# Optimization experiments

Hardware: AMD Instinct MI355X
Metric: run time of the kernel (lower is better)

Reference implementation:

```python
import jax, jax.numpy as jnp
import numpy as np
from jax.ops import segment_sum, segment_max

ALPHA = 0.01  # leaky relu slope

def _cmul(a, b):
    # complex multiply on last-axis (re, im) pairs
    re = a[..., 0] * b[..., 0] - a[..., 1] * b[..., 1]
    im = a[..., 0] * b[..., 1] + a[..., 1] * b[..., 0]
    return jnp.stack((re, im), axis=-1)

def setup_inputs() -> dict:
    key = jax.random.key(0)
    ks = jax.random.split(key, 8)
    N, D, M, E, L, H, R, FH = 50000, 64, 3, 100000, 4, 8, 5, 128
    return {
        "features": jax.random.normal(ks[0], (N, D), jnp.float32),
        "attn1_w": jax.random.normal(ks[1], (M, H, D), jnp.float32) * 0.1,
        "attn2":   jax.random.normal(ks[2], (M, H, D), jnp.float32) * 0.1,
        "r_vec":   jax.random.normal(ks[3], (R, D // 2, 2), jnp.float32),
        "proj_w1": jax.random.normal(ks[4], (FH, H * D), jnp.float32) * 0.05,
        "proj_b1": jnp.zeros((FH,), jnp.float32),
        "proj_w2": jax.random.normal(ks[5], (1, FH), jnp.float32) * 0.1,
        "inst":    jax.random.randint(ks[6], (M, E, L), 0, N),
        "etypes":  jax.random.randint(ks[7], (M, L - 1), 0, 2 * R, dtype=jnp.int32),
    }

def reference(features, attn1_w, attn2, r_vec, proj_w1, proj_b1, proj_w2, inst, etypes):
    N, D = features.shape
    M, E, L = inst.shape
    H = attn1_w.shape[1]
    # --- conjugate-augmented, L2-normalized relation rotations ([2R, D/2, 2]) ---
    rn = r_vec / jnp.linalg.norm(r_vec, axis=2, keepdims=True)
    conj = rn * jnp.array([1.0, -1.0], rn.dtype)
    r_full = jnp.stack((rn, conj), axis=1).reshape(2 * r_vec.shape[0], r_vec.shape[1], 2)

    node_embs = []  # per-metapath [N, H*D]
    for m in range(M):
        # SemanticEncoder: gather + rotation recurrence + mean over path positions
        edata = features[inst[m]]                       # [E, L, D]
        edc = edata.reshape(E, L, D // 2, 2)
        # final_r_vec: backward cumulative complex product; position L-1 = identity
        ident = jnp.concatenate(
            [jnp.ones((D // 2, 1), edata.dtype), jnp.zeros((D // 2, 1), edata.dtype)], axis=-1)
        fr = [None] * L
        fr[L - 1] = ident
        for i in range(L - 2, -1, -1):
            fr[i] = _cmul(fr[i + 1], r_full[etypes[m, i]])
        fr = jnp.stack(fr, axis=0)                      # [L, D/2, 2]
        rotated = _cmul(edc, fr[None])                  # [E, L, D/2, 2] (pos L-1 rotated by identity)
        me = rotated.reshape(E, L, D).mean(axis=1)      # metapath embedding [E, D]

        # MessageAggregator: GAT-style segment softmax over instances per dst node
        dst = inst[m, :, 0]                             # [E]
        a1 = features[dst] @ attn1_w[m].T               # [E, H]
        a2 = jnp.einsum('ed,hd->eh', me, attn2[m])      # [E, H]
        a = jax.nn.leaky_relu(a1 + a2, ALPHA)           # [E, H]
        amax = segment_max(a, dst, num_segments=N)      # [N, H]
        amax = jnp.where(jnp.isfinite(amax), amax, 0.0)
        ex = jnp.exp(a - amax[dst])                     # [E, H]
        den = segment_sum(ex, dst, num_segments=N)      # [N, H]
        attn = ex / jnp.where(den[dst] > 0, den[dst], 1.0)
        agg = segment_sum(attn[:, :, None] * me[:, None, :], dst, num_segments=N)  # [N, H, D]
        node_embs.append(jax.nn.elu(agg).reshape(N, H * D))

    # Subgraph_Fusion: semantic attention over metapaths
    z = jnp.stack(node_embs, axis=1)                    # [N, M, H*D]
    w = jnp.tanh(z @ proj_w1.T + proj_b1) @ proj_w2.T   # [N, M, 1]
    beta = jax.nn.softmax(w.mean(axis=0), axis=0)       # [M, 1]
    out = (beta[None] * z).sum(axis=1)                  # [N, H*D]
    return out
```

## Files before the change

### kernel.cpp

```cpp
#include <hip/hip_runtime.h>
#include <hip/hip_bf16.h>
#include <hip/hip_fp16.h>
#include <math.h>

#define NN 50000
#define DD 64
#define MM 3
#define EE 100000
#define LL 4
#define HH 8
#define FHH 128
#define HD 512
#define NROWS (NN*MM)
#define LRELU_ALPHA 0.01f

#define WSUM_BINS 256
#define WSUM_SZ (MM*WSUM_BINS)
#define BINS (MM*NN)
#define NBLK ((BINS + 1023)/1024)
#define GT_TILE 224

#define OFF_ZB    0
#define OFF_WSUM  (NROWS*HD/2)
#define OFF_BETA  (OFF_WSUM + WSUM_SZ)
#define OFF_W1BF  (OFF_BETA + 16)
#define OFF_WU    (OFF_W1BF + 32768)
#define OFF_FRS   (OFF_WU + 6144)
#define OFF_GT    (OFF_FRS + 768)
#define OFF_INTS  (OFF_GT + MM*NN*32)
#define IOFF_CNT    0
#define IOFF_CURSOR (IOFF_CNT + BINS)
#define IOFF_PART   (IOFF_CURSOR + BINS)
#define IOFF_BSUM   (IOFF_PART + BINS)
#define IOFF_BTOP   (IOFF_BSUM + 256)
#define IOFF_SEGC   (IOFF_BTOP + 256)
#define IOFF_REC    (IOFF_SEGC + 2*BINS)
#define INTS_END    (IOFF_REC + 4*MM*EE)
#define OFF_F16   (OFF_INTS + INTS_END)

typedef short v8s __attribute__((ext_vector_type(8)));
typedef float v4f __attribute__((ext_vector_type(4)));

__device__ __forceinline__ float elu_f(float x) {
    return x > 0.f ? x : (__expf(x) - 1.f);
}

__device__ __forceinline__ float tanh_fast(float x) {
    float e = __expf(2.f * x);
    return 1.f - 2.f / (e + 1.f);
}

__device__ __forceinline__ unsigned int pk_bf16x2(float x, float y) {
    float2 f2; f2.x = x; f2.y = y;
    __hip_bfloat162 h = __float22bfloat162_rn(f2);
    union { __hip_bfloat162 h; unsigned int u; } cv;
    cv.h = h;
    return cv.u;
}

__device__ __forceinline__ float bf_lo(unsigned int u) {
    union { unsigned int x; float f; } c; c.x = u << 16; return c.f;
}
__device__ __forceinline__ float bf_hi(unsigned int u) {
    union { unsigned int x; float f; } c; c.x = u & 0xffff0000u; return c.f;
}

__device__ __forceinline__ float2 h2f(unsigned int u) {
    union { unsigned int x; __half2 h; } c; c.x = u;
    return __half22float2(c.h);
}

__device__ __forceinline__ void build_frs(
    float frs[LL][DD/2][2], const float* r_vec, const int* etypes, int m, int t)
{
    if (t < DD/2) {
        float cr = 1.f, ci = 0.f;
        frs[LL-1][t][0] = 1.f; frs[LL-1][t][1] = 0.f;
        for (int i = LL-2; i >= 0; --i) {
            int et = etypes[m*(LL-1) + i];
            float rr = r_vec[((et>>1)*(DD/2) + t)*2 + 0];
            float ri = r_vec[((et>>1)*(DD/2) + t)*2 + 1];
            float inv = rsqrtf(rr*rr + ri*ri);
            rr *= inv; ri *= inv;
            if (et & 1) ri = -ri;
            float nr = cr*rr - ci*ri;
            float ni = cr*ri + ci*rr;
            cr = nr; ci = ni;
            frs[i][t][0] = cr; frs[i][t][1] = ci;
        }
    }
}

__global__ __launch_bounds__(256) void fcvt_kernel(
    const float* __restrict__ f, ushort* __restrict__ f16)
{
    int i = blockIdx.x*256 + threadIdx.x;
    float4 v = ((const float4*)f)[i];
    __half2 h0 = __float22half2_rn(make_float2(v.x, v.y));
    __half2 h1 = __float22half2_rn(make_float2(v.z, v.w));
    union { __half2 h; unsigned int u; } c0, c1;
    c0.h = h0; c1.h = h1;
    ((uint2*)f16)[i] = make_uint2(c0.u, c1.u);
}


__global__ __launch_bounds__(256) void hist_kernel(
    const int* __restrict__ inst, int* __restrict__ cnt)
{
    int e = blockIdx.x*256 + threadIdx.x;
    int m = blockIdx.y;
    if (e >= EE) return;
    int dst = inst[((size_t)m*EE + e)*LL];
    atomicAdd(&cnt[m*NN + dst], 1);
}

__global__ __launch_bounds__(256) void scan_partial_kernel(
    const int* __restrict__ cnt, int* __restrict__ part, int* __restrict__ bsum)
{
    __shared__ int sd[256];
    const int t = threadIdx.x;
    const int base = blockIdx.x*1024 + t*4;
    int v0=0,v1=0,v2=0,v3=0;
    if (base+3 < BINS) {
        int4 v = *(const int4*)&cnt[base];
        v0=v.x; v1=v.y; v2=v.z; v3=v.w;
    } else {
        if (base+0 < BINS) v0 = cnt[base+0];
        if (base+1 < BINS) v1 = cnt[base+1];
        if (base+2 < BINS) v2 = cnt[base+2];
        if (base+3 < BINS) v3 = cnt[base+3];
    }
    int tot = v0+v1+v2+v3;
    sd[t] = tot; __syncthreads();
    #pragma unroll
    for (int off = 1; off < 256; off <<= 1) {
        int val = (t >= off) ? sd[t-off] : 0;
        __syncthreads();
        sd[t] += val;
        __syncthreads();
    }
    int excl = sd[t] - tot;
    if (base+0 < BINS) part[base+0] = excl;
    if (base+1 < BINS) part[base+1] = excl + v0;
    if (base+2 < BINS) part[base+2] = excl + v0 + v1;
    if (base+3 < BINS) part[base+3] = excl + v0 + v1 + v2;
    if (t == 255) bsum[blockIdx.x] = sd[255];
}

__global__ __launch_bounds__(256) void scan_tops_kernel(
    const int* __restrict__ bsum, int* __restrict__ btop)
{
    __shared__ int sd[256];
    const int t = threadIdx.x;
    int v = (t < NBLK) ? bsum[t] : 0;
    sd[t] = v; __syncthreads();
    #pragma unroll
    for (int off = 1; off < 256; off <<= 1) {
        int val = (t >= off) ? sd[t-off] : 0;
        __syncthreads();
        sd[t] += val;
        __syncthreads();
    }
    if (t < NBLK) btop[t] = sd[t] - v;
}

__global__ __launch_bounds__(256) void fixup_kernel(
    int* __restrict__ part, const int* __restrict__ btop,
    const int* __restrict__ cnt, int2* __restrict__ segc)
{
    int i = blockIdx.x*256 + threadIdx.x;
    if (i >= BINS) return;
    int p = part[i] + btop[i >> 10];
    part[i] = p;
    segc[i] = make_int2(p, cnt[i]);
}

__global__ __launch_bounds__(256) void scatter_kernel(
    const int4* __restrict__ inst4, const int* __restrict__ part,
    int* __restrict__ cursor, int4* __restrict__ rec)
{
    int e = blockIdx.x*256 + threadIdx.x;
    int m = blockIdx.y;
    if (e >= EE) return;
    int4 v = inst4[(size_t)m*EE + e];
    int bin = m*NN + v.x;
    int pos = part[bin] + atomicAdd(&cursor[bin], 1);
    rec[pos] = make_int4(v.y, v.z, v.w, 0);
}

__global__ __launch_bounds__(64) void ugen_kernel(
    const float* __restrict__ r_vec,
    const int* __restrict__ etypes,
    const float* __restrict__ attn1_w,
    const float* __restrict__ attn2,
    float* __restrict__ Wu,
    float* __restrict__ frs_pk)
{
    const int m = blockIdx.x;
    __shared__ float frs[LL][DD/2][2];
    const int t = threadIdx.x;
    build_frs(frs, r_vec, etypes, m, t);
    __syncthreads();
    if (t < 32) {
        float4 v0, v1;
        v0.x = frs[0][t][0]; v0.y = frs[0][t][1];
        v0.z = frs[1][t][0]; v0.w = frs[1][t][1];
        v1.x = frs[2][t][0]; v1.y = frs[2][t][1];
        v1.z = frs[3][t][0]; v1.w = frs[3][t][1];
        ((float4*)frs_pk)[(m*32 + t)*2 + 0] = v0;
        ((float4*)frs_pk)[(m*32 + t)*2 + 1] = v1;
    }
    for (int idx = t; idx < 32*64; idx += 64) {
        int j = idx >> 6, d = idx & 63, p = d >> 1;
        int l = (j < 8) ? 0 : (j >> 3);
        int h = j & 7;
        float fr = frs[l][p][0], fi = frs[l][p][1];
        float w2r = attn2[m*HD + h*DD + 2*p];
        float w2i = attn2[m*HD + h*DD + 2*p + 1];
        float u = (d & 1) ? (fr*w2i - fi*w2r) : (fr*w2r + fi*w2i);
        float val = 0.25f * u + ((j < 8) ? attn1_w[m*HD + h*DD + d] : 0.f);
        Wu[(m*32 + j)*64 + d] = val;
    }
}

__global__ __launch_bounds__(256) void gt_kernel(
    const float* __restrict__ features,
    const float* __restrict__ Wu,
    float* __restrict__ gt)
{
    __shared__ float xs[GT_TILE*65];
    const int m = blockIdx.y;
    const int node0 = blockIdx.x * GT_TILE;
    const int t = threadIdx.x;
    #pragma unroll
    for (int i = 0; i < 14; ++i) {
        int idx = t + 256*i;
        int r = idx >> 4, c4 = idx & 15;
        int gr = node0 + r;
        float4 v = make_float4(0.f,0.f,0.f,0.f);
        if (gr < NN) v = ((const float4*)features)[gr*16 + c4];
        float* dst = &xs[r*65 + c4*4];
        dst[0]=v.x; dst[1]=v.y; dst[2]=v.z; dst[3]=v.w;
    }
    __syncthreads();
    if (t >= GT_TILE) return;
    int node = node0 + t;
    float acc[32];
    #pragma unroll
    for (int j=0;j<32;++j) acc[j]=0.f;
    const float* Wm = Wu + m*2048;
    for (int d = 0; d < 64; ++d) {
        float x = xs[t*65 + d];
        #pragma unroll
        for (int j = 0; j < 32; ++j)
            acc[j] += x * Wm[j*64 + d];
    }
    if (node < NN) {
        float* o = gt + ((size_t)m*NN + node)*32;
        #pragma unroll
        for (int j4 = 0; j4 < 8; ++j4) {
            float4 v; v.x=acc[j4*4]; v.y=acc[j4*4+1]; v.z=acc[j4*4+2]; v.w=acc[j4*4+3];
            ((float4*)o)[j4] = v;
        }
    }
}

__global__ __launch_bounds__(256) void node_kernel(
    const unsigned int* __restrict__ f16u,
    const float* __restrict__ frs_pk,
    const int4*  __restrict__ rec4,
    const int2*  __restrict__ segc,
    const float* __restrict__ gt,
    ushort* __restrict__ Zb)
{
    const int m = blockIdx.y;
    const int t = threadIdx.x;
    const int lane = t & 63;
    const int hl   = lane & 31;
    const int half = lane >> 5;
    const int wid  = t >> 6;
    const int node = blockIdx.x*4 + wid;

    const int bin = m*NN + node;
    ushort* zrow = Zb + ((size_t)node*MM + m)*HD;
    const int2 sc = segc[bin];
    const int start = sc.x, ecnt = sc.y;
    if (ecnt == 0) {
        ((uint4*)zrow)[lane] = make_uint4(0u,0u,0u,0u);
        return;
    }

    const float4* fp = (const float4*)frs_pk + ((size_t)m*32 + hl)*2;
    const float4 fA = fp[0], fB = fp[1];
    const float f0x=fA.x, f0y=fA.y, f1x=fA.z, f1y=fA.w;
    const float f2x=fB.x, f2y=fB.y, f3x=fB.z, f3y=fB.w;

    float2 x0 = h2f(f16u[(size_t)node*32 + hl]);
    const float me0r = x0.x*f0x - x0.y*f0y;
    const float me0i = x0.x*f0y + x0.y*f0x;

    const float c0 = (hl < HH) ? gt[(size_t)bin*32 + hl] : 0.f;
    const int lsel = hl >> 3;
    const bool gm = (hl >= 8);
    const float* gtm = gt + (size_t)m*NN*32;

    float accr[HH], acci[HH];
    #pragma unroll
    for (int h = 0; h < HH; ++h) { accr[h] = 0.f; acci[h] = 0.f; }
    float den = 0.f;

    for (int q = 0; q < ecnt; q += 2) {
        int myq = q + half;
        bool valid = (myq < ecnt);
        int qq = valid ? myq : (ecnt - 1);
        int4 r = rec4[start + qq];
        int i1 = r.x, i2 = r.y, i3 = r.z;

        int idxg = (lsel == 1) ? i1 : ((lsel == 2) ? i2 : i3);
        float gv = 0.f;
        if (gm) gv = gtm[(size_t)idxg*32 + hl];

        unsigned int u1 = f16u[(size_t)i1*32 + hl];
        unsigned int u2 = f16u[(size_t)i2*32 + hl];
        unsigned int u3 = f16u[(size_t)i3*32 + hl];

        gv += __shfl_xor(gv, 16);
        gv += __shfl_xor(gv, 8);

        float2 x1 = h2f(u1), x2 = h2f(u2), x3 = h2f(u3);
        float mer = me0r, mei = me0i;
        mer += x1.x*f1x - x1.y*f1y;  mei += x1.x*f1y + x1.y*f1x;
        mer += x2.x*f2x - x2.y*f2y;  mei += x2.x*f2y + x2.y*f2x;
        mer += x3.x*f3x - x3.y*f3y;  mei += x3.x*f3y + x3.y*f3x;
        mer *= 0.25f; mei *= 0.25f;

        float ex = 0.f;
        if (hl < HH) {
            float a = c0 + gv;
            a = a > 0.f ? a : LRELU_ALPHA*a;
            ex = valid ? __expf(a) : 0.f;
            den += ex;
        }
        #pragma unroll
        for (int h = 0; h < HH; ++h) {
            float e = __shfl(ex, (lane & 32) + h);
            accr[h] += e * mer;
            acci[h] += e * mei;
        }
    }

    #pragma unroll
    for (int h = 0; h < HH; ++h) {
        accr[h] += __shfl_xor(accr[h], 32);
        acci[h] += __shfl_xor(acci[h], 32);
    }
    den += __shfl_xor(den, 32);

    const int hbase = half ? 4 : 0;
    #pragma unroll
    for (int hh = 0; hh < 4; ++hh) {
        int h = hbase + hh;
        float dh = __shfl(den, h);
        float inv = __builtin_amdgcn_rcpf(dh);
        float vr = elu_f(accr[h] * inv);
        float vi = elu_f(acci[h] * inv);
        ((unsigned int*)zrow)[h*32 + hl] = pk_bf16x2(vr, vi);
    }
}


__global__ __launch_bounds__(64) void cvt_w1_kernel(
    const float* __restrict__ w1, ushort* __restrict__ w1bf)
{
    int i = blockIdx.x*64 + threadIdx.x;
    float4 v = ((const float4*)w1)[i];
    uint2 p;
    p.x = pk_bf16x2(v.x, v.y);
    p.y = pk_bf16x2(v.z, v.w);
    ((uint2*)w1bf)[i] = p;
}

__global__ __launch_bounds__(256,3) void wproj_kernel(
    const ushort* __restrict__ Zb,
    const ushort* __restrict__ w1bf,
    const float* __restrict__ b1,
    const float* __restrict__ w2,
    float* __restrict__ wsum)
{
    __shared__ ushort As[128*72];
    __shared__ ushort Bs[128*72];
    __shared__ float wacc[MM];
    const int t = threadIdx.x;
    const int row0 = blockIdx.x * 128;
    if (t < MM) wacc[t] = 0.f;
    const int lane = t & 63;
    const int wid  = t >> 6;
    const int ln   = lane & 15;
    const int quad = lane >> 4;
    const int wr   = wid >> 1;
    const int wc   = wid & 1;

    v4f acc[4][4];
    #pragma unroll
    for (int i=0;i<4;++i)
        #pragma unroll
        for (int j=0;j<4;++j)
            acc[i][j] = (v4f){0.f,0.f,0.f,0.f};

    const uint4* zb4 = (const uint4*)Zb;
    const uint4* wb4 = (const uint4*)w1bf;

    for (int kt = 0; kt < 8; ++kt) {
        __syncthreads();
        #pragma unroll
        for (int i = 0; i < 4; ++i) {
            int idx = t + 256*i;
            int r = idx >> 3, k8 = idx & 7;
            int gr = row0 + r;
            uint4 v = make_uint4(0u,0u,0u,0u);
            if (gr < NROWS) v = zb4[(size_t)gr*64 + kt*8 + k8];
            *(uint4*)&As[r*72 + k8*8] = v;
        }
        #pragma unroll
        for (int i = 0; i < 4; ++i) {
            int idx = t + 256*i;
            int f = idx >> 3, k8 = idx & 7;
            uint4 v = wb4[f*64 + kt*8 + k8];
            *(uint4*)&Bs[f*72 + k8*8] = v;
        }
        __syncthreads();
        #pragma unroll
        for (int kk = 0; kk < 2; ++kk) {
            v8s a[4], b[4];
            #pragma unroll
            for (int i=0;i<4;++i)
                a[i] = *(const v8s*)&As[(wr*64 + i*16 + ln)*72 + kk*32 + quad*8];
            #pragma unroll
            for (int j=0;j<4;++j)
                b[j] = *(const v8s*)&Bs[(wc*64 + j*16 + ln)*72 + kk*32 + quad*8];
            #pragma unroll
            for (int i=0;i<4;++i)
                #pragma unroll
                for (int j=0;j<4;++j)
                    acc[i][j] = __builtin_amdgcn_mfma_f32_16x16x32_bf16(
                        a[i], b[j], acc[i][j], 0, 0, 0);
        }
    }

    float b1v[4], w2v[4];
    #pragma unroll
    for (int j=0;j<4;++j) {
        int col = wc*64 + j*16 + ln;
        b1v[j] = b1[col];
        w2v[j] = w2[col];
    }
    #pragma unroll
    for (int i=0;i<4;++i) {
        #pragma unroll
        for (int reg=0;reg<4;++reg) {
            float s = 0.f;
            #pragma unroll
            for (int j=0;j<4;++j)
                s += tanh_fast(acc[i][j][reg] + b1v[j]) * w2v[j];
            s += __shfl_xor(s, 1);
            s += __shfl_xor(s, 2);
            s += __shfl_xor(s, 4);
            s += __shfl_xor(s, 8);
            int grow = row0 + wr*64 + i*16 + quad*4 + reg;
            if (ln == 0 && grow < NROWS)
                atomicAdd(&wacc[grow % MM], s);
        }
    }
    __syncthreads();
    if (t < MM)
        atomicAdd(&wsum[t*WSUM_BINS + (blockIdx.x & (WSUM_BINS-1))], wacc[t]);
}

__global__ void beta_kernel(const float* __restrict__ wsum, float* __restrict__ beta)
{
    __shared__ float sm[MM];
    int t = threadIdx.x;
    if (t < MM) {
        float s = 0.f;
        for (int i = 0; i < WSUM_BINS; ++i) s += wsum[t*WSUM_BINS + i];
        sm[t] = s / (float)NN;
    }
    __syncthreads();
    if (t < MM) {
        float a = sm[0], b = sm[1], c = sm[2];
        float mx = fmaxf(a, fmaxf(b, c));
        float e0 = __expf(a-mx), e1 = __expf(b-mx), e2 = __expf(c-mx);
        float tot = e0+e1+e2;
        float mine = (t==0?e0:(t==1?e1:e2));
        beta[t] = mine/tot;
    }
}

__global__ __launch_bounds__(256) void out_kernel(
    const ushort* __restrict__ Zb, const float* __restrict__ beta,
    float* __restrict__ out)
{
    int i = blockIdx.x*256 + threadIdx.x;
    int n  = i >> 6;
    int jj = i & 63;
    float b0 = beta[0], b1v = beta[1], b2 = beta[2];
    const uint4* zb4 = (const uint4*)Zb;
    uint4 v0 = zb4[((size_t)n*MM + 0)*64 + jj];
    uint4 v1 = zb4[((size_t)n*MM + 1)*64 + jj];
    uint4 v2 = zb4[((size_t)n*MM + 2)*64 + jj];
    float o[8];
    o[0] = b0*bf_lo(v0.x) + b1v*bf_lo(v1.x) + b2*bf_lo(v2.x);
    o[1] = b0*bf_hi(v0.x) + b1v*bf_hi(v1.x) + b2*bf_hi(v2.x);
    o[2] = b0*bf_lo(v0.y) + b1v*bf_lo(v1.y) + b2*bf_lo(v2.y);
    o[3] = b0*bf_hi(v0.y) + b1v*bf_hi(v1.y) + b2*bf_hi(v2.y);
    o[4] = b0*bf_lo(v0.z) + b1v*bf_lo(v1.z) + b2*bf_lo(v2.z);
    o[5] = b0*bf_hi(v0.z) + b1v*bf_hi(v1.z) + b2*bf_hi(v2.z);
    o[6] = b0*bf_lo(v0.w) + b1v*bf_lo(v1.w) + b2*bf_lo(v2.w);
    o[7] = b0*bf_hi(v0.w) + b1v*bf_hi(v1.w) + b2*bf_hi(v2.w);
    float4* op = (float4*)(out + (size_t)n*HD + jj*8);
    op[0] = make_float4(o[0],o[1],o[2],o[3]);
    op[1] = make_float4(o[4],o[5],o[6],o[7]);
}

extern "C" void kernel_launch(void* const* d_in, const int* in_sizes, int n_in,
                              void* d_out, int out_size, void* d_ws, size_t ws_size,
                              hipStream_t stream) {
    const float* features = (const float*)d_in[0];
    const float* attn1_w  = (const float*)d_in[1];
    const float* attn2    = (const float*)d_in[2];
    const float* r_vec    = (const float*)d_in[3];
    const float* proj_w1  = (const float*)d_in[4];
    const float* proj_b1  = (const float*)d_in[5];
    const float* proj_w2  = (const float*)d_in[6];
    const int*   inst     = (const int*)d_in[7];
    const int*   etypes   = (const int*)d_in[8];
    float* out = (float*)d_out;

    float* ws    = (float*)d_ws;
    ushort* Zb   = (ushort*)(ws + OFF_ZB);
    float* wsum  = ws + OFF_WSUM;
    float* beta  = ws + OFF_BETA;
    ushort* w1bf = (ushort*)(ws + OFF_W1BF);
    float* Wu    = ws + OFF_WU;
    float* frs_pk= ws + OFF_FRS;
    float* gt    = ws + OFF_GT;
    int* ints    = (int*)(ws + OFF_INTS);
    int* cnt     = ints + IOFF_CNT;
    int* cursor  = ints + IOFF_CURSOR;
    int* part    = ints + IOFF_PART;
    int* bsum    = ints + IOFF_BSUM;
    int* btop    = ints + IOFF_BTOP;
    int2* segc   = (int2*)(ints + IOFF_SEGC);
    int4* rec4   = (int4*)(ints + IOFF_REC);
    ushort* f16  = (ushort*)(ws + OFF_F16);

    hipMemsetAsync(cnt, 0, (size_t)2*BINS*sizeof(int), stream);
    hipMemsetAsync(wsum, 0, (size_t)WSUM_SZ*sizeof(float), stream);

    fcvt_kernel<<<NN*DD/4/256, 256, 0, stream>>>(features, f16);
    cvt_w1_kernel<<<256, 64, 0, stream>>>(proj_w1, w1bf);
    ugen_kernel<<<MM, 64, 0, stream>>>(r_vec, etypes, attn1_w, attn2, Wu, frs_pk);
    gt_kernel<<<dim3((NN + GT_TILE-1)/GT_TILE, MM), 256, 0, stream>>>(features, Wu, gt);
    hist_kernel<<<dim3((EE+255)/256, MM), 256, 0, stream>>>(inst, cnt);
    scan_partial_kernel<<<NBLK, 256, 0, stream>>>(cnt, part, bsum);
    scan_tops_kernel<<<1, 256, 0, stream>>>(bsum, btop);
    fixup_kernel<<<(BINS+255)/256, 256, 0, stream>>>(part, btop, cnt, segc);
    scatter_kernel<<<dim3((EE+255)/256, MM), 256, 0, stream>>>(
        (const int4*)inst, part, cursor, rec4);
    node_kernel<<<dim3(NN/4, MM), 256, 0, stream>>>(
        (const unsigned int*)f16, frs_pk, rec4, segc, gt, Zb);
    wproj_kernel<<<(NROWS + 127)/128, 256, 0, stream>>>(Zb, w1bf, proj_b1, proj_w2, wsum);
    beta_kernel<<<1, 64, 0, stream>>>(wsum, beta);
    out_kernel<<<NN*64/256, 256, 0, stream>>>(Zb, beta, out);
}
```

Measured before the change: 382.9 us.

## Merge preprocessing kernels and switch node aggregation to packed half2 math

Folds the small preprocessing launches (feature and weight conversion, rotation/weight generation, histogram, wsum zeroing) into one multi-role kernel. It also merges the gt projection with the partial scan, and the offset fixup with the scatter, which cuts the launch count from about 13 to 8. Inside node_kernel, the complex rotation and the attention-weighted accumulation now use packed half2 FMAs with pre-scaled, pre-packed rotation coefficients instead of fp32. This lowers ALU work but accumulates per-head sums in fp16, which adds precision and overflow risk for nodes with many instances.

```diff
diff --git a/kernel.cpp b/kernel.cpp
--- a/kernel.cpp
+++ b/kernel.cpp
@@ -19,6 +19,20 @@
 #define BINS (MM*NN)
 #define NBLK ((BINS + 1023)/1024)
 #define GT_TILE 224
+
+#define FCVT_B 3125
+#define CW1_B  64
+#define UGEN_B 3
+#define HISTG  392
+#define HIST_B (HISTG*MM)
+#define PREP_B (FCVT_B + CW1_B + UGEN_B + HIST_B + 1)
+
+#define GT_B   (224*MM)
+#define MID_B  (GT_B + NBLK)
+
+#define SCAT_B (HISTG*MM)
+#define SEGC_B ((BINS + 255)/256)
+#define SCT_B  (SCAT_B + SEGC_B)
 
 #define OFF_ZB    0
 #define OFF_WSUM  (NROWS*HD/2)
@@ -58,6 +72,13 @@
     return cv.u;
 }
 
+__device__ __forceinline__ unsigned int pk_h2(float x, float y) {
+    __half2 h = __floats2half2_rn(x, y);
+    union { __half2 h; unsigned int u; } cv;
+    cv.h = h;
+    return cv.u;
+}
+
 __device__ __forceinline__ float bf_lo(unsigned int u) {
     union { unsigned int x; float f; } c; c.x = u << 16; return c.f;
 }
@@ -65,9 +86,14 @@
     union { unsigned int x; float f; } c; c.x = u & 0xffff0000u; return c.f;
 }
 
-__device__ __forceinline__ float2 h2f(unsigned int u) {
-    union { unsigned int x; __half2 h; } c; c.x = u;
-    return __half22float2(c.h);
+__device__ __forceinline__ __half2 u2h(unsigned int u) {
+    union { unsigned int x; __half2 h; } c; c.x = u; return c.h;
+}
+__device__ __forceinline__ unsigned int h2u(__half2 h) {
+    union { __half2 h; unsigned int x; } c; c.h = h; return c.x;
+}
+__device__ __forceinline__ unsigned int swp(unsigned int u) {
+    return (u >> 16) | (u << 16);
 }
 
 __device__ __forceinline__ void build_frs(
@@ -91,47 +117,151 @@
     }
 }
 
-__global__ __launch_bounds__(256) void fcvt_kernel(
-    const float* __restrict__ f, ushort* __restrict__ f16)
-{
-    int i = blockIdx.x*256 + threadIdx.x;
-    float4 v = ((const float4*)f)[i];
-    __half2 h0 = __float22half2_rn(make_float2(v.x, v.y));
-    __half2 h1 = __float22half2_rn(make_float2(v.z, v.w));
-    union { __half2 h; unsigned int u; } c0, c1;
-    c0.h = h0; c1.h = h1;
-    ((uint2*)f16)[i] = make_uint2(c0.u, c1.u);
-}
-
-
-__global__ __launch_bounds__(256) void hist_kernel(
-    const int* __restrict__ inst, int* __restrict__ cnt)
-{
-    int e = blockIdx.x*256 + threadIdx.x;
-    int m = blockIdx.y;
-    if (e >= EE) return;
-    int dst = inst[((size_t)m*EE + e)*LL];
-    atomicAdd(&cnt[m*NN + dst], 1);
-}
-
-__global__ __launch_bounds__(256) void scan_partial_kernel(
-    const int* __restrict__ cnt, int* __restrict__ part, int* __restrict__ bsum)
+__global__ __launch_bounds__(256) void prep_kernel(
+    const float* __restrict__ features, ushort* __restrict__ f16,
+    const float* __restrict__ w1, ushort* __restrict__ w1bf,
+    const float* __restrict__ r_vec, const int* __restrict__ etypes,
+    const float* __restrict__ attn1_w, const float* __restrict__ attn2,
+    float* __restrict__ Wu, unsigned int* __restrict__ frs_h,
+    const int* __restrict__ inst, int* __restrict__ cnt,
+    float* __restrict__ wsum)
+{
+    const int b = blockIdx.x;
+    const int t = threadIdx.x;
+    if (b < FCVT_B) {
+        int i = b*256 + t;
+        float4 v = ((const float4*)features)[i];
+        ((uint2*)f16)[i] = make_uint2(pk_h2(v.x, v.y), pk_h2(v.z, v.w));
+    } else if (b < FCVT_B + CW1_B) {
+        int i = (b - FCVT_B)*256 + t;
+        float4 v = ((const float4*)w1)[i];
+        uint2 p; p.x = pk_bf16x2(v.x, v.y); p.y = pk_bf16x2(v.z, v.w);
+        ((uint2*)w1bf)[i] = p;
+    } else if (b < FCVT_B + CW1_B + UGEN_B) {
+        const int m = b - (FCVT_B + CW1_B);
+        __shared__ float frs[LL][DD/2][2];
+        build_frs(frs, r_vec, etypes, m, t);
+        __syncthreads();
+        if (t < 32) {
+            unsigned int vals[8];
+            #pragma unroll
+            for (int l = 0; l < LL; ++l) {
+                float fr = 0.25f * frs[l][t][0];
+                float fi = 0.25f * frs[l][t][1];
+                vals[2*l+0] = pk_h2(fr, fr);
+                vals[2*l+1] = pk_h2(-fi, fi);
+            }
+            uint4* dst = (uint4*)frs_h + (m*32 + t)*2;
+            dst[0] = make_uint4(vals[0], vals[1], vals[2], vals[3]);
+            dst[1] = make_uint4(vals[4], vals[5], vals[6], vals[7]);
+        }
+        for (int idx = t; idx < 32*64; idx += 256) {
+            int j = idx >> 6, d = idx & 63, p = d >> 1;
+            int l = (j < 8) ? 0 : (j >> 3);
+            int h = j & 7;
+            float fr = frs[l][p][0], fi = frs[l][p][1];
+            float w2r = attn2[m*HD + h*DD + 2*p];
+            float w2i = attn2[m*HD + h*DD + 2*p + 1];
+            float u = (d & 1) ? (fr*w2i - fi*w2r) : (fr*w2r + fi*w2i);
+            float val = 0.25f * u + ((j < 8) ? attn1_w[m*HD + h*DD + d] : 0.f);
+            Wu[(m*32 + j)*64 + d] = val;
+        }
+    } else if (b < FCVT_B + CW1_B + UGEN_B + HIST_B) {
+        int idx = b - (FCVT_B + CW1_B + UGEN_B);
+        int m = idx / HISTG;
+        int e = (idx - m*HISTG)*256 + t;
+        if (e < EE) {
+            int dst = inst[((size_t)m*EE + e)*LL];
+            atomicAdd(&cnt[m*NN + dst], 1);
+        }
+    } else {
+        for (int i = t; i < WSUM_SZ; i += 256) wsum[i] = 0.f;
+    }
+}
+
+__global__ __launch_bounds__(256) void mid_kernel(
+    const float* __restrict__ features,
+    const float* __restrict__ Wu,
+    float* __restrict__ gt,
+    const int* __restrict__ cnt,
+    int* __restrict__ part, int* __restrict__ bsum)
+{
+    __shared__ float xs[GT_TILE*65];
+    __shared__ int sd[256];
+    const int b = blockIdx.x;
+    const int t = threadIdx.x;
+    if (b < GT_B) {
+        const int m = b / 224;
+        const int node0 = (b - m*224) * GT_TILE;
+        #pragma unroll
+        for (int i = 0; i < 14; ++i) {
+            int idx = t + 256*i;
+            int r = idx >> 4, c4 = idx & 15;
+            int gr = node0 + r;
+            float4 v = make_float4(0.f,0.f,0.f,0.f);
+            if (gr < NN) v = ((const float4*)features)[gr*16 + c4];
+            float* dst = &xs[r*65 + c4*4];
+            dst[0]=v.x; dst[1]=v.y; dst[2]=v.z; dst[3]=v.w;
+        }
+        __syncthreads();
+        if (t >= GT_TILE) return;
+        int node = node0 + t;
+        float acc[32];
+        #pragma unroll
+        for (int j=0;j<32;++j) acc[j]=0.f;
+        const float* Wm = Wu + m*2048;
+        for (int d = 0; d < 64; ++d) {
+            float x = xs[t*65 + d];
+            #pragma unroll
+            for (int j = 0; j < 32; ++j)
+                acc[j] += x * Wm[j*64 + d];
+        }
+        if (node < NN) {
+            float* o = gt + ((size_t)m*NN + node)*32;
+            #pragma unroll
+            for (int j4 = 0; j4 < 8; ++j4) {
+                float4 v; v.x=acc[j4*4]; v.y=acc[j4*4+1]; v.z=acc[j4*4+2]; v.w=acc[j4*4+3];
+                ((float4*)o)[j4] = v;
+            }
+        }
+    } else {
+        const int bb = b - GT_B;
+        const int base = bb*1024 + t*4;
+        int v0=0,v1=0,v2=0,v3=0;
+        if (base+3 < BINS) {
+            int4 v = *(const int4*)&cnt[base];
+            v0=v.x; v1=v.y; v2=v.z; v3=v.w;
+        } else {
+            if (base+0 < BINS) v0 = cnt[base+0];
+            if (base+1 < BINS) v1 = cnt[base+1];
+            if (base+2 < BINS) v2 = cnt[base+2];
+            if (base+3 < BINS) v3 = cnt[base+3];
+        }
+        int tot = v0+v1+v2+v3;
+        sd[t] = tot; __syncthreads();
+        #pragma unroll
+        for (int off = 1; off < 256; off <<= 1) {
+            int val = (t >= off) ? sd[t-off] : 0;
+            __syncthreads();
+            sd[t] += val;
+            __syncthreads();
+        }
+        int excl = sd[t] - tot;
+        if (base+0 < BINS) part[base+0] = excl;
+        if (base+1 < BINS) part[base+1] = excl + v0;
+        if (base+2 < BINS) part[base+2] = excl + v0 + v1;
+        if (base+3 < BINS) part[base+3] = excl + v0 + v1 + v2;
+        if (t == 255) bsum[bb] = sd[255];
+    }
+}
+
+__global__ __launch_bounds__(256) void scan_tops_kernel(
+    const int* __restrict__ bsum, int* __restrict__ btop)
 {
     __shared__ int sd[256];
     const int t = threadIdx.x;
-    const int base = blockIdx.x*1024 + t*4;
-    int v0=0,v1=0,v2=0,v3=0;
-    if (base+3 < BINS) {
-        int4 v = *(const int4*)&cnt[base];
-        v0=v.x; v1=v.y; v2=v.z; v3=v.w;
-    } else {
-        if (base+0 < BINS) v0 = cnt[base+0];
-        if (base+1 < BINS) v1 = cnt[base+1];
-        if (base+2 < BINS) v2 = cnt[base+2];
-        if (base+3 < BINS) v3 = cnt[base+3];
-    }
-    int tot = v0+v1+v2+v3;
-    sd[t] = tot; __syncthreads();
+    int v = (t < NBLK) ? bsum[t] : 0;
+    sd[t] = v; __syncthreads();
     #pragma unroll
     for (int off = 1; off < 256; off <<= 1) {
         int val = (t >= off) ? sd[t-off] : 0;
@@ -139,135 +269,35 @@
         sd[t] += val;
         __syncthreads();
     }
-    int excl = sd[t] - tot;
-    if (base+0 < BINS) part[base+0] = excl;
-    if (base+1 < BINS) part[base+1] = excl + v0;
-    if (base+2 < BINS) part[base+2] = excl + v0 + v1;
-    if (base+3 < BINS) part[base+3] = excl + v0 + v1 + v2;
-    if (t == 255) bsum[blockIdx.x] = sd[255];
-}
-
-__global__ __launch_bounds__(256) void scan_tops_kernel(
-    const int* __restrict__ bsum, int* __restrict__ btop)
-{
-    __shared__ int sd[256];
+    if (t < NBLK) btop[t] = sd[t] - v;
+}
+
+__global__ __launch_bounds__(256) void scat_kernel(
+    const int4* __restrict__ inst4, const int* __restrict__ part,
+    const int* __restrict__ btop, int* __restrict__ cursor,
+    int4* __restrict__ rec, const int* __restrict__ cnt,
+    int2* __restrict__ segc)
+{
+    const int b = blockIdx.x;
     const int t = threadIdx.x;
-    int v = (t < NBLK) ? bsum[t] : 0;
-    sd[t] = v; __syncthreads();
-    #pragma unroll
-    for (int off = 1; off < 256; off <<= 1) {
-        int val = (t >= off) ? sd[t-off] : 0;
-        __syncthreads();
-        sd[t] += val;
-        __syncthreads();
-    }
-    if (t < NBLK) btop[t] = sd[t] - v;
-}
-
-__global__ __launch_bounds__(256) void fixup_kernel(
-    int* __restrict__ part, const int* __restrict__ btop,
-    const int* __restrict__ cnt, int2* __restrict__ segc)
-{
-    int i = blockIdx.x*256 + threadIdx.x;
-    if (i >= BINS) return;
-    int p = part[i] + btop[i >> 10];
-    part[i] = p;
-    segc[i] = make_int2(p, cnt[i]);
-}
-
-__global__ __launch_bounds__(256) void scatter_kernel(
-    const int4* __restrict__ inst4, const int* __restrict__ part,
-    int* __restrict__ cursor, int4* __restrict__ rec)
-{
-    int e = blockIdx.x*256 + threadIdx.x;
-    int m = blockIdx.y;
-    if (e >= EE) return;
-    int4 v = inst4[(size_t)m*EE + e];
-    int bin = m*NN + v.x;
-    int pos = part[bin] + atomicAdd(&cursor[bin], 1);
-    rec[pos] = make_int4(v.y, v.z, v.w, 0);
-}
-
-__global__ __launch_bounds__(64) void ugen_kernel(
-    const float* __restrict__ r_vec,
-    const int* __restrict__ etypes,
-    const float* __restrict__ attn1_w,
-    const float* __restrict__ attn2,
-    float* __restrict__ Wu,
-    float* __restrict__ frs_pk)
-{
-    const int m = blockIdx.x;
-    __shared__ float frs[LL][DD/2][2];
-    const int t = threadIdx.x;
-    build_frs(frs, r_vec, etypes, m, t);
-    __syncthreads();
-    if (t < 32) {
-        float4 v0, v1;
-        v0.x = frs[0][t][0]; v0.y = frs[0][t][1];
-        v0.z = frs[1][t][0]; v0.w = frs[1][t][1];
-        v1.x = frs[2][t][0]; v1.y = frs[2][t][1];
-        v1.z = frs[3][t][0]; v1.w = frs[3][t][1];
-        ((float4*)frs_pk)[(m*32 + t)*2 + 0] = v0;
-        ((float4*)frs_pk)[(m*32 + t)*2 + 1] = v1;
-    }
-    for (int idx = t; idx < 32*64; idx += 64) {
-        int j = idx >> 6, d = idx & 63, p = d >> 1;
-        int l = (j < 8) ? 0 : (j >> 3);
-        int h = j & 7;
-        float fr = frs[l][p][0], fi = frs[l][p][1];
-        float w2r = attn2[m*HD + h*DD + 2*p];
-        float w2i = attn2[m*HD + h*DD + 2*p + 1];
-        float u = (d & 1) ? (fr*w2i - fi*w2r) : (fr*w2r + fi*w2i);
-        float val = 0.25f * u + ((j < 8) ? attn1_w[m*HD + h*DD + d] : 0.f);
-        Wu[(m*32 + j)*64 + d] = val;
-    }
-}
-
-__global__ __launch_bounds__(256) void gt_kernel(
-    const float* __restrict__ features,
-    const float* __restrict__ Wu,
-    float* __restrict__ gt)
-{
-    __shared__ float xs[GT_TILE*65];
-    const int m = blockIdx.y;
-    const int node0 = blockIdx.x * GT_TILE;
-    const int t = threadIdx.x;
-    #pragma unroll
-    for (int i = 0; i < 14; ++i) {
-        int idx = t + 256*i;
-        int r = idx >> 4, c4 = idx & 15;
-        int gr = node0 + r;
-        float4 v = make_float4(0.f,0.f,0.f,0.f);
-        if (gr < NN) v = ((const float4*)features)[gr*16 + c4];
-        float* dst = &xs[r*65 + c4*4];
-        dst[0]=v.x; dst[1]=v.y; dst[2]=v.z; dst[3]=v.w;
-    }
-    __syncthreads();
-    if (t >= GT_TILE) return;
-    int node = node0 + t;
-    float acc[32];
-    #pragma unroll
-    for (int j=0;j<32;++j) acc[j]=0.f;
-    const float* Wm = Wu + m*2048;
-    for (int d = 0; d < 64; ++d) {
-        float x = xs[t*65 + d];
-        #pragma unroll
-        for (int j = 0; j < 32; ++j)
-            acc[j] += x * Wm[j*64 + d];
-    }
-    if (node < NN) {
-        float* o = gt + ((size_t)m*NN + node)*32;
-        #pragma unroll
-        for (int j4 = 0; j4 < 8; ++j4) {
-            float4 v; v.x=acc[j4*4]; v.y=acc[j4*4+1]; v.z=acc[j4*4+2]; v.w=acc[j4*4+3];
-            ((float4*)o)[j4] = v;
-        }
+    if (b < SCAT_B) {
+        int m = b / HISTG;
+        int e = (b - m*HISTG)*256 + t;
+        if (e >= EE) return;
+        int4 v = inst4[(size_t)m*EE + e];
+        int bin = m*NN + v.x;
+        int pos = part[bin] + btop[bin >> 10] + atomicAdd(&cursor[bin], 1);
+        rec[pos] = make_int4(v.y, v.z, v.w, 0);
+    } else {
+        int i = (b - SCAT_B)*256 + t;
+        if (i < BINS)
+            segc[i] = make_int2(part[i] + btop[i >> 10], cnt[i]);
     }
 }
 
 __global__ __launch_bounds__(256) void node_kernel(
     const unsigned int* __restrict__ f16u,
-    const float* __restrict__ frs_pk,
+    const unsigned int* __restrict__ frs_h,
     const int4*  __restrict__ rec4,
     const int2*  __restrict__ segc,
     const float* __restrict__ gt,
@@ -290,23 +320,21 @@
         return;
     }
 
-    const float4* fp = (const float4*)frs_pk + ((size_t)m*32 + hl)*2;
-    const float4 fA = fp[0], fB = fp[1];
-    const float f0x=fA.x, f0y=fA.y, f1x=fA.z, f1y=fA.w;
-    const float f2x=fB.x, f2y=fB.y, f3x=fB.z, f3y=fB.w;
-
-    float2 x0 = h2f(f16u[(size_t)node*32 + hl]);
-    const float me0r = x0.x*f0x - x0.y*f0y;
-    const float me0i = x0.x*f0y + x0.y*f0x;
+    const uint4* fh = (const uint4*)frs_h + ((size_t)(m*32 + hl))*2;
+    const uint4 ca = fh[0], cb = fh[1];
+
+    const unsigned int ux0 = f16u[(size_t)node*32 + hl];
+    const __half2 me0 = __hfma2(u2h(swp(ux0)), u2h(ca.y),
+                                __hmul2(u2h(ux0), u2h(ca.x)));
 
     const float c0 = (hl < HH) ? gt[(size_t)bin*32 + hl] : 0.f;
     const int lsel = hl >> 3;
     const bool gm = (hl >= 8);
     const float* gtm = gt + (size_t)m*NN*32;
 
-    float accr[HH], acci[HH];
-    #pragma unroll
-    for (int h = 0; h < HH; ++h) { accr[h] = 0.f; acci[h] = 0.f; }
+    __half2 acc[HH];
+    #pragma unroll
+    for (int h = 0; h < HH; ++h) acc[h] = u2h(0u);
     float den = 0.f;
 
     for (int q = 0; q < ecnt; q += 2) {
@@ -327,32 +355,31 @@
         gv += __shfl_xor(gv, 16);
         gv += __shfl_xor(gv, 8);
 
-        float2 x1 = h2f(u1), x2 = h2f(u2), x3 = h2f(u3);
-        float mer = me0r, mei = me0i;
-        mer += x1.x*f1x - x1.y*f1y;  mei += x1.x*f1y + x1.y*f1x;
-        mer += x2.x*f2x - x2.y*f2y;  mei += x2.x*f2y + x2.y*f2x;
-        mer += x3.x*f3x - x3.y*f3y;  mei += x3.x*f3y + x3.y*f3x;
-        mer *= 0.25f; mei *= 0.25f;
-
-        float ex = 0.f;
-        if (hl < HH) {
-            float a = c0 + gv;
-            a = a > 0.f ? a : LRELU_ALPHA*a;
-            ex = valid ? __expf(a) : 0.f;
-            den += ex;
-        }
+        __half2 me = me0;
+        me = __hfma2(u2h(u1), u2h(ca.z), me);
+        me = __hfma2(u2h(swp(u1)), u2h(ca.w), me);
+        me = __hfma2(u2h(u2), u2h(cb.x), me);
+        me = __hfma2(u2h(swp(u2)), u2h(cb.y), me);
+        me = __hfma2(u2h(u3), u2h(cb.z), me);
+        me = __hfma2(u2h(swp(u3)), u2h(cb.w), me);
+
+        float a = c0 + gv;
+        a = a > 0.f ? a : LRELU_ALPHA*a;
+        float ex = valid ? __expf(a) : 0.f;
+        den += ex;
+        unsigned int exu = h2u(__float2half2_rn(ex));
+
         #pragma unroll
         for (int h = 0; h < HH; ++h) {
-            float e = __shfl(ex, (lane & 32) + h);
-            accr[h] += e * mer;
-            acci[h] += e * mei;
+            unsigned int eu = __shfl(exu, (lane & 32) + h);
+            acc[h] = __hfma2(u2h(eu), me, acc[h]);
         }
     }
 
     #pragma unroll
     for (int h = 0; h < HH; ++h) {
-        accr[h] += __shfl_xor(accr[h], 32);
-        acci[h] += __shfl_xor(acci[h], 32);
+        unsigned int au = __shfl_xor(h2u(acc[h]), 32);
+        acc[h] = __hadd2(acc[h], u2h(au));
     }
     den += __shfl_xor(den, 32);
 
@@ -360,25 +387,16 @@
     #pragma unroll
     for (int hh = 0; hh < 4; ++hh) {
         int h = hbase + hh;
+        unsigned int sel = half ? h2u(acc[hh+4]) : h2u(acc[hh]);
         float dh = __shfl(den, h);
         float inv = __builtin_amdgcn_rcpf(dh);
-        float vr = elu_f(accr[h] * inv);
-        float vi = elu_f(acci[h] * inv);
+        float2 v = __half22float2(u2h(sel));
+        float vr = elu_f(v.x * inv);
+        float vi = elu_f(v.y * inv);
         ((unsigned int*)zrow)[h*32 + hl] = pk_bf16x2(vr, vi);
     }
 }
 
-
-__global__ __launch_bounds__(64) void cvt_w1_kernel(
-    const float* __restrict__ w1, ushort* __restrict__ w1bf)
-{
-    int i = blockIdx.x*64 + threadIdx.x;
-    float4 v = ((const float4*)w1)[i];
-    uint2 p;
-    p.x = pk_bf16x2(v.x, v.y);
-    p.y = pk_bf16x2(v.z, v.w);
-    ((uint2*)w1bf)[i] = p;
-}
 
 __global__ __launch_bounds__(256,3) void wproj_kernel(
     const ushort* __restrict__ Zb,
@@ -542,7 +560,7 @@
     float* beta  = ws + OFF_BETA;
     ushort* w1bf = (ushort*)(ws + OFF_W1BF);
     float* Wu    = ws + OFF_WU;
-    float* frs_pk= ws + OFF_FRS;
+    unsigned int* frs_h = (unsigned int*)(ws + OFF_FRS);
     float* gt    = ws + OFF_GT;
     int* ints    = (int*)(ws + OFF_INTS);
     int* cnt     = ints + IOFF_CNT;
@@ -555,20 +573,16 @@
     ushort* f16  = (ushort*)(ws + OFF_F16);
 
     hipMemsetAsync(cnt, 0, (size_t)2*BINS*sizeof(int), stream);
-    hipMemsetAsync(wsum, 0, (size_t)WSUM_SZ*sizeof(float), stream);
-
-    fcvt_kernel<<<NN*DD/4/256, 256, 0, stream>>>(features, f16);
-    cvt_w1_kernel<<<256, 64, 0, stream>>>(proj_w1, w1bf);
-    ugen_kernel<<<MM, 64, 0, stream>>>(r_vec, etypes, attn1_w, attn2, Wu, frs_pk);
-    gt_kernel<<<dim3((NN + GT_TILE-1)/GT_TILE, MM), 256, 0, stream>>>(features, Wu, gt);
-    hist_kernel<<<dim3((EE+255)/256, MM), 256, 0, stream>>>(inst, cnt);
-    scan_partial_kernel<<<NBLK, 256, 0, stream>>>(cnt, part, bsum);
+
+    prep_kernel<<<PREP_B, 256, 0, stream>>>(
+        features, f16, proj_w1, w1bf, r_vec, etypes, attn1_w, attn2,
+        Wu, frs_h, inst, cnt, wsum);
+    mid_kernel<<<MID_B, 256, 0, stream>>>(features, Wu, gt, cnt, part, bsum);
     scan_tops_kernel<<<1, 256, 0, stream>>>(bsum, btop);
-    fixup_kernel<<<(BINS+255)/256, 256, 0, stream>>>(part, btop, cnt, segc);
-    scatter_kernel<<<dim3((EE+255)/256, MM), 256, 0, stream>>>(
-        (const int4*)inst, part, cursor, rec4);
+    scat_kernel<<<SCT_B, 256, 0, stream>>>(
+        (const int4*)inst, part, btop, cursor, rec4, cnt, segc);
     node_kernel<<<dim3(NN/4, MM), 256, 0, stream>>>(
-        (const unsigned int*)f16, frs_pk, rec4, segc, gt, Zb);
+        (const unsigned int*)f16, frs_h, rec4, segc, gt, Zb);
     wproj_kernel<<<(NROWS + 127)/128, 256, 0, stream>>>(Zb, w1bf, proj_b1, proj_w2, wsum);
     beta_kernel<<<1, 64, 0, stream>>>(wsum, beta);
     out_kernel<<<NN*64/256, 256, 0, stream>>>(Zb, beta, out);
```

Result: faster. 354.3 us (-7.5%).
